# Performance work log

Hardware: AMD Instinct MI355X
Metric: run time of the kernel (lower is better)

The kernel has to match this reference:

```python
import jax, jax.numpy as jnp
import numpy as np

B, C, N, K, C_OUT = 4, 64, 8192, 16, 64


def setup_inputs() -> dict:
    key = jax.random.key(0)
    k1, k2, k3, k4 = jax.random.split(key, 4)
    x = jax.random.normal(k1, (B, C, N, 1), dtype=jnp.float32)
    edge_index = jax.random.randint(k2, (2, B, N, K), 0, N, dtype=jnp.int64)
    # 1x1 conv weights of BasicConv([2C, C_OUT]) -> [C_OUT, 2C]
    W = jax.random.normal(k3, (C_OUT, 2 * C), dtype=jnp.float32) * (1.0 / np.sqrt(2 * C))
    b = jax.random.normal(k4, (C_OUT,), dtype=jnp.float32) * 0.01
    return {"x": x, "edge_index": edge_index, "W": W, "b": b}


def _batched_index_select(x, idx):
    # x: [B, C, N] ; idx: [B, N, K] -> [B, C, N, K]
    b, c, n = x.shape
    k = idx.shape[-1]
    flat = jnp.broadcast_to(idx.reshape(b, 1, n * k), (b, c, n * k))
    return jnp.take_along_axis(x, flat, axis=2).reshape(b, c, n, k)


def reference(x, edge_index, W, b):
    xs = x[..., 0]                                  # [B, C, N]
    x_i = _batched_index_select(xs, edge_index[1])  # [B, C, N, K] central nodes
    x_j = _batched_index_select(xs, edge_index[0])  # [B, C, N, K] neighbors
    feat = jnp.concatenate([x_i, x_j - x_i], axis=1)  # [B, 2C, N, K]
    # 1x1 conv: [C_OUT, 2C] x [B, 2C, N, K] -> [B, C_OUT, N, K], + bias, ReLU (norm=None)
    h = jnp.einsum('oc,bcnk->bonk', W, feat) + b[None, :, None, None]
    h = jax.nn.relu(h)
    # max over neighbors, keepdim on last axis -> [B, C_OUT, N, 1]
    return jnp.max(h, axis=-1, keepdims=True)
```

## Files before the change

### kernel.cpp

```cpp
#include <hip/hip_runtime.h>


#define BB   4
#define CCH  64
#define NN   8192
#define KK   16

typedef _Float16 h2  __attribute__((ext_vector_type(2)));
typedef _Float16 h8  __attribute__((ext_vector_type(8)));
typedef _Float16 h16 __attribute__((ext_vector_type(16)));
typedef int      v4i __attribute__((ext_vector_type(4)));

#if __has_builtin(__builtin_amdgcn_fdot2)
#define FDOT2(a, b, c) __builtin_amdgcn_fdot2((a), (b), (c), false)
#else
#define FDOT2(a, b, c) ((c) + (float)(a).x * (float)(b).x + (float)(a).y * (float)(b).y)
#endif

__global__ __launch_bounds__(256) void gemm_kernel(const float* __restrict__ x,
                                                   const float* __restrict__ W,
                                                   _Float16* __restrict__ y) {
    __shared__ _Float16 wT2[32 * 264];
    __shared__ _Float16 xs2[32 * 264];

    const int t   = threadIdx.x;
    const int blk = blockIdx.x;
    const int b   = blk >> 6;
    const int n0  = (blk & 63) * 128;

    {
        const int k  = t & 63;
        const int kp = k >> 1, par = k & 1;
        const int sb = t >> 6;
        #pragma unroll
        for (int i = 0; i < 32; ++i) {
            const int s = sb + 4 * i;
            float v;
            if (s < CCH) v = W[s * 128 + k] - W[s * 128 + 64 + k];
            else         v = W[(s - CCH) * 128 + 64 + k];
            wT2[kp * 264 + 2 * s + par] = (_Float16)v;
        }
    }
    {
        const float* xb = x + (size_t)b * CCH * NN + n0;
        #pragma unroll
        for (int i = 0; i < 8; ++i) {
            const int k  = (t >> 5) + 8 * i;
            const int nq = (t & 31) * 4;
            const float4 v = *(const float4*)&xb[(size_t)k * NN + nq];
            const int kp = k >> 1, par = k & 1;
            _Float16* d = &xs2[kp * 264 + 2 * nq + par];
            d[0] = (_Float16)v.x; d[2] = (_Float16)v.y;
            d[4] = (_Float16)v.z; d[6] = (_Float16)v.w;
        }
    }
    __syncthreads();

    const int sg = t & 15;
    const int ng = t >> 4;
    const int s0 = sg * 8, nn0 = ng * 8;

    float acc[8][8];
    #pragma unroll
    for (int i = 0; i < 8; ++i)
        #pragma unroll
        for (int j = 0; j < 8; ++j) acc[i][j] = 0.f;

    #pragma unroll 2
    for (int kp = 0; kp < 32; ++kp) {
        const h16 wv = *(const h16*)&wT2[kp * 264 + 2 * s0];
        const h16 xv = *(const h16*)&xs2[kp * 264 + 2 * nn0];
        #pragma unroll
        for (int i = 0; i < 8; ++i) {
            h2 wp; wp.x = wv[2 * i]; wp.y = wv[2 * i + 1];
            #pragma unroll
            for (int j = 0; j < 8; ++j) {
                h2 xp; xp.x = xv[2 * j]; xp.y = xv[2 * j + 1];
                acc[i][j] = FDOT2(wp, xp, acc[i][j]);
            }
        }
    }

    _Float16* yb = y + ((size_t)b * NN + n0 + nn0) * 128 + s0;
    #pragma unroll
    for (int j = 0; j < 8; ++j) {
        h8 v;
        #pragma unroll
        for (int i = 0; i < 8; ++i) v[i] = (_Float16)acc[i][j];
        *(h8*)&yb[(size_t)j * 128] = v;
    }
}

__global__ __launch_bounds__(256) void gather_kernel(const _Float16* __restrict__ y,
                                                     const int* __restrict__ edge,
                                                     const float* __restrict__ bias,
                                                     float* __restrict__ out) {
    __shared__ int   eL[16][2][16];
    __shared__ float so[16][65];

    const int t   = threadIdx.x;
    const int blk = blockIdx.x;
    const int xcd  = blk & 7;
    const int b    = xcd >> 1;
    const int tile = ((blk >> 3) << 1) | (xcd & 1);
    const int n0   = tile * 16;

    if (t < 128) {
        const int src = t >> 6;
        const int f   = (t & 63) << 2;
        const int nl  = f >> 4, k0 = f & 15;
        const size_t eb = (size_t)(src == 0 ? BB + b : b) * NN * KK;
        *(v4i*)&eL[nl][src][k0] = *(const v4i*)&edge[eb + (size_t)(n0 + nl) * KK + k0];
    }
    __syncthreads();

    const int w    = t >> 6;
    const int lane = t & 63;
    const int half = lane >> 5;
    const int cl   = lane & 31;

    const float2 bv = *(const float2*)&bias[2 * cl];
    const _Float16* yb = y + (size_t)b * NN * 128;

    #pragma unroll 2
    for (int u = 0; u < 4; ++u) {
        const int nl = 4 * w + u;
        h2 s[8];
        #pragma unroll
        for (int kp = 0; kp < 8; ++kp) {
            const int k  = 2 * kp + half;
            const int i1 = eL[nl][0][k];
            const int i0 = eL[nl][1][k];
            const uint a = *(const uint*)&yb[(size_t)i1 * 128 + 2 * cl];
            const uint c = *(const uint*)&yb[(size_t)i0 * 128 + 64 + 2 * cl];
            union { uint u32; h2 h; } ua, uc;
            ua.u32 = a; uc.u32 = c;
            s[kp] = ua.h + uc.h;
        }
        h2 m = s[0];
        #pragma unroll
        for (int kp = 1; kp < 8; ++kp) m = __builtin_elementwise_max(m, s[kp]);
        union { int i32; h2 h; } um, uo;
        um.h = m;
        uo.i32 = __shfl_xor(um.i32, 32, 64);
        m = __builtin_elementwise_max(m, uo.h);
        if (half == 0) {
            float2 r;
            r.x = fmaxf((float)m.x + bv.x, 0.f);
            r.y = fmaxf((float)m.y + bv.y, 0.f);
            *(float2*)&so[nl][2 * cl] = r;
        }
    }
    __syncthreads();

    {
        const int c = t >> 2;
        const int q = t & 3;
        float4 v;
        v.x = so[4 * q + 0][c];
        v.y = so[4 * q + 1][c];
        v.z = so[4 * q + 2][c];
        v.w = so[4 * q + 3][c];
        *(float4*)(out + ((size_t)b * CCH + c) * NN + n0 + 4 * q) = v;
    }
}

extern "C" void kernel_launch(void* const* d_in, const int* in_sizes, int n_in,
                              void* d_out, int out_size, void* d_ws, size_t ws_size,
                              hipStream_t stream) {
    (void)in_sizes; (void)n_in; (void)out_size; (void)ws_size;
    const float* x    = (const float*)d_in[0];
    const int*   edge = (const int*)d_in[1];
    const float* W    = (const float*)d_in[2];
    const float* bias = (const float*)d_in[3];
    float*       out  = (float*)d_out;
    _Float16*    y    = (_Float16*)d_ws;

    gemm_kernel<<<dim3(256), dim3(256), 0, stream>>>(x, W, y);
    gather_kernel<<<dim3(2048), dim3(256), 0, stream>>>(y, edge, bias, out);
}
```

Baseline: 27.20 us.

## Widen gather loads to 16-byte vectors and process 32 nodes per block

The gather kernel now has each lane fetch 8 halfs (16 bytes) per neighbor row instead of 2, with 8 neighbor groups per wave reduced by xor-shuffles across lanes. Each block handles 32 nodes instead of 16, which halves the grid, and the XCD-aware block-to-batch mapping is replaced by a simple linear mapping. The goal is fewer, wider memory transactions and more loads in flight per thread to cut gather latency. In exchange it adds shuffle-reduction work, raises register pressure, and drops the XCD locality mapping.

```diff
diff --git a/kernel.cpp b/kernel.cpp
--- a/kernel.cpp
+++ b/kernel.cpp
@@ -95,72 +95,86 @@
                                                      const int* __restrict__ edge,
                                                      const float* __restrict__ bias,
                                                      float* __restrict__ out) {
-    __shared__ int   eL[16][2][16];
-    __shared__ float so[16][65];
+    __shared__ int   eL[32][2][16];
+    __shared__ float sm[32][68];
 
     const int t   = threadIdx.x;
     const int blk = blockIdx.x;
-    const int xcd  = blk & 7;
-    const int b    = xcd >> 1;
-    const int tile = ((blk >> 3) << 1) | (xcd & 1);
-    const int n0   = tile * 16;
+    const int b   = blk >> 8;
+    const int n0  = (blk & 255) * 32;
 
-    if (t < 128) {
-        const int src = t >> 6;
-        const int f   = (t & 63) << 2;
-        const int nl  = f >> 4, k0 = f & 15;
-        const size_t eb = (size_t)(src == 0 ? BB + b : b) * NN * KK;
-        *(v4i*)&eL[nl][src][k0] = *(const v4i*)&edge[eb + (size_t)(n0 + nl) * KK + k0];
+    {
+        const int e   = t << 2;
+        const int n   = e >> 5;
+        const int src = (e >> 4) & 1;
+        const int k0  = e & 15;
+        const size_t ebase = (size_t)(src == 0 ? BB + b : b) * NN * KK;
+        *(v4i*)&eL[n][src][k0] = *(const v4i*)&edge[ebase + (size_t)(n0 + n) * KK + k0];
     }
     __syncthreads();
 
     const int w    = t >> 6;
     const int lane = t & 63;
-    const int half = lane >> 5;
-    const int cl   = lane & 31;
+    const int kg   = lane >> 3;
+    const int cs   = lane & 7;
 
-    const float2 bv = *(const float2*)&bias[2 * cl];
     const _Float16* yb = y + (size_t)b * NN * 128;
+    const float4 bv0 = *(const float4*)&bias[cs * 8];
+    const float4 bv1 = *(const float4*)&bias[cs * 8 + 4];
 
-    #pragma unroll 2
-    for (int u = 0; u < 4; ++u) {
-        const int nl = 4 * w + u;
-        h2 s[8];
+    #pragma unroll
+    for (int batch = 0; batch < 2; ++batch) {
+        h8 a1[4], a2[4], c1[4], c2[4];
         #pragma unroll
-        for (int kp = 0; kp < 8; ++kp) {
-            const int k  = 2 * kp + half;
-            const int i1 = eL[nl][0][k];
-            const int i0 = eL[nl][1][k];
-            const uint a = *(const uint*)&yb[(size_t)i1 * 128 + 2 * cl];
-            const uint c = *(const uint*)&yb[(size_t)i0 * 128 + 64 + 2 * cl];
-            union { uint u32; h2 h; } ua, uc;
-            ua.u32 = a; uc.u32 = c;
-            s[kp] = ua.h + uc.h;
+        for (int u = 0; u < 4; ++u) {
+            const int nn  = w * 8 + batch * 4 + u;
+            const int i1a = eL[nn][0][kg];
+            const int i1b = eL[nn][0][kg + 8];
+            const int i0a = eL[nn][1][kg];
+            const int i0b = eL[nn][1][kg + 8];
+            a1[u] = *(const h8*)&yb[(size_t)i1a * 128 + cs * 8];
+            a2[u] = *(const h8*)&yb[(size_t)i1b * 128 + cs * 8];
+            c1[u] = *(const h8*)&yb[(size_t)i0a * 128 + 64 + cs * 8];
+            c2[u] = *(const h8*)&yb[(size_t)i0b * 128 + 64 + cs * 8];
         }
-        h2 m = s[0];
         #pragma unroll
-        for (int kp = 1; kp < 8; ++kp) m = __builtin_elementwise_max(m, s[kp]);
-        union { int i32; h2 h; } um, uo;
-        um.h = m;
-        uo.i32 = __shfl_xor(um.i32, 32, 64);
-        m = __builtin_elementwise_max(m, uo.h);
-        if (half == 0) {
-            float2 r;
-            r.x = fmaxf((float)m.x + bv.x, 0.f);
-            r.y = fmaxf((float)m.y + bv.y, 0.f);
-            *(float2*)&so[nl][2 * cl] = r;
+        for (int u = 0; u < 4; ++u) {
+            const int nn = w * 8 + batch * 4 + u;
+            union { h8 v; int i[4]; } um, ut;
+            um.v = __builtin_elementwise_max(a1[u] + c1[u], a2[u] + c2[u]);
+            #pragma unroll
+            for (int s = 8; s < 64; s <<= 1) {
+                #pragma unroll
+                for (int r = 0; r < 4; ++r) ut.i[r] = __shfl_xor(um.i[r], s, 64);
+                um.v = __builtin_elementwise_max(um.v, ut.v);
+            }
+            if (kg == 0) {
+                float4 ra, rb;
+                ra.x = fmaxf((float)um.v[0] + bv0.x, 0.f);
+                ra.y = fmaxf((float)um.v[1] + bv0.y, 0.f);
+                ra.z = fmaxf((float)um.v[2] + bv0.z, 0.f);
+                ra.w = fmaxf((float)um.v[3] + bv0.w, 0.f);
+                rb.x = fmaxf((float)um.v[4] + bv1.x, 0.f);
+                rb.y = fmaxf((float)um.v[5] + bv1.y, 0.f);
+                rb.z = fmaxf((float)um.v[6] + bv1.z, 0.f);
+                rb.w = fmaxf((float)um.v[7] + bv1.w, 0.f);
+                *(float4*)&sm[nn][cs * 8]     = ra;
+                *(float4*)&sm[nn][cs * 8 + 4] = rb;
+            }
         }
     }
     __syncthreads();
 
-    {
-        const int c = t >> 2;
-        const int q = t & 3;
+    #pragma unroll
+    for (int r2 = 0; r2 < 2; ++r2) {
+        const int idx = t + (r2 << 8);
+        const int c   = idx >> 3;
+        const int q   = idx & 7;
         float4 v;
-        v.x = so[4 * q + 0][c];
-        v.y = so[4 * q + 1][c];
-        v.z = so[4 * q + 2][c];
-        v.w = so[4 * q + 3][c];
+        v.x = sm[4 * q + 0][c];
+        v.y = sm[4 * q + 1][c];
+        v.z = sm[4 * q + 2][c];
+        v.w = sm[4 * q + 3][c];
         *(float4*)(out + ((size_t)b * CCH + c) * NN + n0 + 4 * q) = v;
     }
 }
@@ -177,5 +191,5 @@
     _Float16*    y    = (_Float16*)d_ws;
 
     gemm_kernel<<<dim3(256), dim3(256), 0, stream>>>(x, W, y);
-    gather_kernel<<<dim3(2048), dim3(256), 0, stream>>>(y, edge, bias, out);
+    gather_kernel<<<dim3(1024), dim3(256), 0, stream>>>(y, edge, bias, out);
 }
```

New measurement: 32.28 us. 18.7% more time.
